# Kernel tuning notes

Measured on AMD Instinct MI355X. Metric: run time of the kernel, lower is better.

The kernel has to match this reference:

```python
import jax, jax.numpy as jnp
import numpy as np

B, S, D, H, WIN = 2, 2048, 1024, 16, 128
DH = D // H


def setup_inputs() -> dict:
    key = jax.random.key(0)
    ks = jax.random.split(key, 6)
    sc = D ** -0.5
    return {
        "x": jax.random.normal(ks[0], (B, S, D), jnp.float32),
        "in_proj_w": jax.random.normal(ks[1], (3 * D, D), jnp.float32) * sc,
        "in_proj_b": jnp.zeros((3 * D,), jnp.float32),
        "out_proj_w": jax.random.normal(ks[2], (D, D), jnp.float32) * sc,
        "out_proj_b": jnp.zeros((D,), jnp.float32),
        "ln1_g": jnp.ones((D,), jnp.float32),
        "ln1_b": jnp.zeros((D,), jnp.float32),
        "spec_wr": jax.random.normal(ks[3], (S // 2 + 1, D), jnp.float32) * 0.02 + 1.0,
        "spec_wi": jax.random.normal(ks[4], (S // 2 + 1, D), jnp.float32) * 0.02,
        "ln2_g": jnp.ones((D,), jnp.float32),
        "ln2_b": jnp.zeros((D,), jnp.float32),
    }


def _layernorm(x, g, b, eps=1e-5):
    mu = jnp.mean(x, axis=-1, keepdims=True)
    var = jnp.mean(jnp.square(x - mu), axis=-1, keepdims=True)
    return (x - mu) * jax.lax.rsqrt(var + eps) * g + b


def reference(x, in_proj_w, in_proj_b, out_proj_w, out_proj_b,
              ln1_g, ln1_b, spec_wr, spec_wi, ln2_g, ln2_b):
    b, s, d = x.shape
    # --- sliding-window MHA (torch nn.MultiheadAttention math) ---
    qkv = x @ in_proj_w.T + in_proj_b            # [B,S,3D]
    q, k, v = jnp.split(qkv, 3, axis=-1)
    q = q.reshape(b, s, H, DH)
    k = k.reshape(b, s, H, DH)
    v = v.reshape(b, s, H, DH)
    scores = jnp.einsum('bqhd,bkhd->bhqk', q, k) * (DH ** -0.5)
    idx = jnp.arange(s)
    band_mask = jnp.abs(idx[:, None] - idx[None, :]) > WIN  # True = masked
    scores = jnp.where(band_mask[None, None], -jnp.inf, scores)
    probs = jax.nn.softmax(scores, axis=-1)
    attn = jnp.einsum('bhqk,bkhd->bqhd', probs, v).reshape(b, s, d)
    attn_out = attn @ out_proj_w.T + out_proj_b
    x_attn = _layernorm(x + attn_out, ln1_g, ln1_b)
    # --- spectral block: rfft along seq, learned complex filter, irfft ---
    Xf = jnp.fft.rfft(x, axis=1)                  # [B, S//2+1, D] complex
    Wc = spec_wr + 1j * spec_wi
    x_wave = jnp.fft.irfft(Xf * Wc[None], n=s, axis=1).astype(x.dtype)
    # --- mix ---
    return _layernorm(x_attn + x_wave, ln2_g, ln2_b)
```

## Files before the change

### kernel.cpp

```cpp
#include <hip/hip_runtime.h>
#include <hip/hip_bf16.h>
#include <math.h>

#define BB    2
#define SS    2048
#define DD    1024
#define HH    16
#define DHH   64
#define WINW  128
#define MROWS (BB * SS)

typedef __attribute__((ext_vector_type(8))) short short8;
typedef __attribute__((ext_vector_type(4))) short short4v;
typedef __attribute__((ext_vector_type(4))) float floatx4;

__device__ __forceinline__ float bf2f(short s) {
  union { unsigned u; float f; } t;
  t.u = ((unsigned)(unsigned short)s) << 16;
  return t.f;
}

__device__ inline void load16_lds(const __hip_bfloat16* g, __hip_bfloat16* l) {
  __builtin_amdgcn_global_load_lds(
      (const __attribute__((address_space(1))) uint32_t*)g,
      (__attribute__((address_space(3))) uint32_t*)l, 16, 0, 0);
}

__global__ __launch_bounds__(256) void prep_fused(
    const float* __restrict__ x, float* __restrict__ xT,
    __hip_bfloat16* __restrict__ x_bf,
    const float* __restrict__ w_in, const float* __restrict__ w_out,
    __hip_bfloat16* __restrict__ w_in_bf, __hip_bfloat16* __restrict__ w_out_bf,
    const float* __restrict__ wr, const float* __restrict__ wi,
    __hip_bfloat16* __restrict__ wrT, __hip_bfloat16* __restrict__ wiT) {
  __shared__ float tile[64][65];
  const int id = blockIdx.x;
  const int tx = threadIdx.x & 63;
  const int ty = threadIdx.x >> 6;

  if (id < 1024) {
    const int bz = id >> 9;
    const int rem = id & 511;
    const int c0 = (rem & 15) * 64;
    const int r0 = (rem >> 4) * 64;
    const size_t base = (size_t)bz * SS * DD;
#pragma unroll
    for (int i = 0; i < 16; ++i) {
      const int r = ty * 16 + i;
      const float v = x[base + (size_t)(r0 + r) * DD + c0 + tx];
      tile[r][tx] = v;
      x_bf[base + (size_t)(r0 + r) * DD + c0 + tx] = __float2bfloat16(v);
    }
    __syncthreads();
#pragma unroll
    for (int i = 0; i < 16; ++i) {
      const int c = ty * 16 + i;
      xT[base + (size_t)(c0 + c) * SS + r0 + tx] = tile[tx][c];
    }
  } else if (id < 2048) {
    const int blk = id - 1024;
    const float* src; __hip_bfloat16* dst; size_t off;
    if (blk < 768) { src = w_in; dst = w_in_bf; off = (size_t)blk * 4096; }
    else { src = w_out; dst = w_out_bf; off = (size_t)(blk - 768) * 4096; }
#pragma unroll
    for (int c = 0; c < 4; ++c) {
      const size_t j = off + c * 1024 + threadIdx.x * 4;
      const float4 v = *(const float4*)(src + j);
      dst[j + 0] = __float2bfloat16(v.x);
      dst[j + 1] = __float2bfloat16(v.y);
      dst[j + 2] = __float2bfloat16(v.z);
      dst[j + 3] = __float2bfloat16(v.w);
    }
  } else {
    const int id2 = id - 2048;
    const int half = id2 >= 272;
    const int rem = id2 - (half ? 272 : 0);
    const float* src = half ? wi : wr;
    __hip_bfloat16* dst = half ? wiT : wrT;
    const int R = 1025, C = DD;
    const int c0 = (rem & 15) * 64;
    const int r0 = (rem >> 4) * 64;
#pragma unroll
    for (int i = 0; i < 16; ++i) {
      const int r = ty * 16 + i;
      if (r0 + r < R) tile[r][tx] = src[(size_t)(r0 + r) * C + c0 + tx];
    }
    __syncthreads();
#pragma unroll
    for (int i = 0; i < 16; ++i) {
      const int c = ty * 16 + i;
      if (r0 + tx < R) dst[(size_t)(c0 + c) * R + r0 + tx] = __float2bfloat16(tile[tx][c]);
    }
  }
}

template <bool BF16OUT>
__device__ __forceinline__ void gemm_tile128(
    const __hip_bfloat16* __restrict__ A, const __hip_bfloat16* __restrict__ B,
    const float* __restrict__ bias, void* __restrict__ Cp,
    int N, int K, int row0, int col0, __hip_bfloat16* sm) {
  __hip_bfloat16* As0 = sm;
  __hip_bfloat16* As1 = sm + 4096;
  __hip_bfloat16* Bs0 = sm + 8192;
  __hip_bfloat16* Bs1 = sm + 12288;
  const int tid  = threadIdx.x;
  const int lane = tid & 63;
  const int wave = tid >> 6;
  const int wrow = (wave >> 1) * 64;
  const int wcol = (wave & 1) * 64;
  const int srow = tid >> 2;
  const int skk  = (tid & 3) * 8;
  const int quad = lane >> 4;
  const int l16  = lane & 15;
  floatx4 acc[4][4] = {};
  for (int k0 = 0; k0 < K; k0 += 64) {
    __syncthreads();
    load16_lds(A + (size_t)(row0 + srow) * K + k0 + skk,           &As0[tid * 8]);
    load16_lds(A + (size_t)(row0 + 64 + srow) * K + k0 + skk,      &As0[2048 + tid * 8]);
    load16_lds(A + (size_t)(row0 + srow) * K + k0 + 32 + skk,      &As1[tid * 8]);
    load16_lds(A + (size_t)(row0 + 64 + srow) * K + k0 + 32 + skk, &As1[2048 + tid * 8]);
    load16_lds(B + (size_t)(col0 + srow) * K + k0 + skk,           &Bs0[tid * 8]);
    load16_lds(B + (size_t)(col0 + 64 + srow) * K + k0 + skk,      &Bs0[2048 + tid * 8]);
    load16_lds(B + (size_t)(col0 + srow) * K + k0 + 32 + skk,      &Bs1[tid * 8]);
    load16_lds(B + (size_t)(col0 + 64 + srow) * K + k0 + 32 + skk, &Bs1[2048 + tid * 8]);
    __syncthreads();
    {
      short8 af[4], bf[4];
#pragma unroll
      for (int i = 0; i < 4; ++i)
        af[i] = *(const short8*)&As0[(wrow + i * 16 + l16) * 32 + quad * 8];
#pragma unroll
      for (int j = 0; j < 4; ++j)
        bf[j] = *(const short8*)&Bs0[(wcol + j * 16 + l16) * 32 + quad * 8];
#pragma unroll
      for (int i = 0; i < 4; ++i)
#pragma unroll
        for (int j = 0; j < 4; ++j)
          acc[i][j] = __builtin_amdgcn_mfma_f32_16x16x32_bf16(af[i], bf[j], acc[i][j], 0, 0, 0);
    }
    {
      short8 af[4], bf[4];
#pragma unroll
      for (int i = 0; i < 4; ++i)
        af[i] = *(const short8*)&As1[(wrow + i * 16 + l16) * 32 + quad * 8];
#pragma unroll
      for (int j = 0; j < 4; ++j)
        bf[j] = *(const short8*)&Bs1[(wcol + j * 16 + l16) * 32 + quad * 8];
#pragma unroll
      for (int i = 0; i < 4; ++i)
#pragma unroll
        for (int j = 0; j < 4; ++j)
          acc[i][j] = __builtin_amdgcn_mfma_f32_16x16x32_bf16(af[i], bf[j], acc[i][j], 0, 0, 0);
    }
  }
#pragma unroll
  for (int i = 0; i < 4; ++i) {
#pragma unroll
    for (int j = 0; j < 4; ++j) {
      const int col = col0 + wcol + j * 16 + l16;
      const float bs = bias[col];
#pragma unroll
      for (int r = 0; r < 4; ++r) {
        const int row = row0 + wrow + i * 16 + quad * 4 + r;
        if (BF16OUT)
          ((__hip_bfloat16*)Cp)[(size_t)row * N + col] = __float2bfloat16(acc[i][j][r] + bs);
        else
          ((float*)Cp)[(size_t)row * N + col] = acc[i][j][r] + bs;
      }
    }
  }
}

#define PAD2(a) ((a) + ((a) >> 5))

__device__ __forceinline__ void spec_body(
    int sid, float* __restrict__ xT,
    const __hip_bfloat16* __restrict__ wrT, const __hip_bfloat16* __restrict__ wiT,
    float* smf) {
  float2* cx  = (float2*)smf;
  float2* twb = cx + 2112;
  float2* twl = twb + 1024;
  const int tid = threadIdx.x;
  const int dpair = sid & 511;
  const int b = sid >> 9;
  const int d0 = dpair * 2, d1 = d0 + 1;
  float* col0 = xT + ((size_t)b * DD + d0) * SS;
  float* col1 = xT + ((size_t)b * DD + d1) * SS;

  for (int s4 = tid * 4; s4 < SS; s4 += 1024) {
    const float4 a = *(const float4*)(col0 + s4);
    const float4 c = *(const float4*)(col1 + s4);
    const int p = PAD2(s4);
    cx[p + 0] = float2{a.x, c.x};
    cx[p + 1] = float2{a.y, c.y};
    cx[p + 2] = float2{a.z, c.z};
    cx[p + 3] = float2{a.w, c.w};
  }
  for (int j = tid; j < 1024; j += 256) {
    float sn, cs;
    __sincosf(-6.283185307179586f * (float)j * (1.0f / 2048.0f), &sn, &cs);
    twb[j] = float2{cs, sn};
  }
#pragma unroll
  for (int s = 1; s <= 9; ++s) {
    const int sz = 1 << (s - 1);
    const float ang = -6.283185307179586f / (float)(1 << s);
    for (int p = tid; p < sz; p += 256) {
      float sn, cs;
      __sincosf(ang * (float)p, &sn, &cs);
      twl[sz - 1 + p] = float2{cs, sn};
    }
  }

  for (int stage = 11; stage >= 1; --stage) {
    __syncthreads();
    const int half = 1 << (stage - 1);
    const float2* twp = (stage >= 10) ? twb : (twl + (half - 1));
    const int tmul = (stage == 10) ? 2 : 1;
#pragma unroll 2
    for (int t = tid; t < SS / 2; t += 256) {
      const int gI = t >> (stage - 1);
      const int p = t & (half - 1);
      const int i = (gI << stage) + p;
      const int j = i + half;
      const float2 w = twp[p * tmul];
      const int ii = PAD2(i), jj = PAD2(j);
      const float2 a = cx[ii];
      const float2 bv = cx[jj];
      cx[ii] = float2{a.x + bv.x, a.y + bv.y};
      const float dr = a.x - bv.x, di = a.y - bv.y;
      cx[jj] = float2{dr * w.x - di * w.y, dr * w.y + di * w.x};
    }
  }
  __syncthreads();

  const __hip_bfloat16* w0r = wrT + (size_t)d0 * 1025;
  const __hip_bfloat16* w0i = wiT + (size_t)d0 * 1025;
  const __hip_bfloat16* w1r = wrT + (size_t)d1 * 1025;
  const __hip_bfloat16* w1i = wiT + (size_t)d1 * 1025;
  const float sc = 1.0f / (float)SS;
  for (int k = tid; k < 1024; k += 256) {
    if (k == 0) {
      const float2 z0 = cx[0];
      cx[0] = float2{z0.x * __bfloat162float(w0r[0]) * sc,
                     z0.y * __bfloat162float(w1r[0]) * sc};
      const float2 zn = cx[1];
      cx[1] = float2{zn.x * __bfloat162float(w0r[1024]) * sc,
                     zn.y * __bfloat162float(w1r[1024]) * sc};
    } else {
      const int p1 = PAD2(__brev((unsigned)k) >> 21);
      const int p2 = PAD2(__brev((unsigned)(SS - k)) >> 21);
      const float2 A = cx[p1];
      const float2 Bv = cx[p2];
      const float z0r = 0.5f * (A.x + Bv.x), z0i = 0.5f * (A.y - Bv.y);
      const float z1r = 0.5f * (A.y + Bv.y), z1i = -0.5f * (A.x - Bv.x);
      const float a0 = __bfloat162float(w0r[k]) * sc, b0 = __bfloat162float(w0i[k]) * sc;
      const float a1 = __bfloat162float(w1r[k]) * sc, b1 = __bfloat162float(w1i[k]) * sc;
      const float y0r = z0r * a0 - z0i * b0, y0i = z0r * b0 + z0i * a0;
      const float y1r = z1r * a1 - z1i * b1, y1i = z1r * b1 + z1i * a1;
      cx[p1] = float2{y0r - y1i, y0i + y1r};
      cx[p2] = float2{y0r + y1i, y1r - y0i};
    }
  }

  for (int stage = 1; stage <= 11; ++stage) {
    __syncthreads();
    const int half = 1 << (stage - 1);
    const float2* twp = (stage >= 10) ? twb : (twl + (half - 1));
    const int tmul = (stage == 10) ? 2 : 1;
#pragma unroll 2
    for (int t = tid; t < SS / 2; t += 256) {
      const int gI = t >> (stage - 1);
      const int p = t & (half - 1);
      const int i = (gI << stage) + p;
      const int j = i + half;
      const float2 w = twp[p * tmul];
      const int ii = PAD2(i), jj = PAD2(j);
      const float2 bv = cx[jj];
      const float tr = bv.x * w.x + bv.y * w.y;
      const float ti = bv.y * w.x - bv.x * w.y;
      const float2 a = cx[ii];
      cx[ii] = float2{a.x + tr, a.y + ti};
      cx[jj] = float2{a.x - tr, a.y - ti};
    }
  }
  __syncthreads();

  for (int s4 = tid * 4; s4 < SS; s4 += 1024) {
    const int p = PAD2(s4);
    float4 a, c;
    const float2 v0 = cx[p + 0], v1 = cx[p + 1], v2 = cx[p + 2], v3 = cx[p + 3];
    a.x = v0.x; a.y = v1.x; a.z = v2.x; a.w = v3.x;
    c.x = v0.y; c.y = v1.y; c.z = v2.y; c.w = v3.y;
    *(float4*)(col0 + s4) = a;
    *(float4*)(col1 + s4) = c;
  }
}

__global__ __launch_bounds__(256) void gemm1_spec(
    const __hip_bfloat16* __restrict__ x_bf, const __hip_bfloat16* __restrict__ w_in_bf,
    const float* __restrict__ in_b, __hip_bfloat16* __restrict__ qkv_bf,
    float* __restrict__ xT, const __hip_bfloat16* __restrict__ wrT,
    const __hip_bfloat16* __restrict__ wiT) {
  extern __shared__ __align__(16) char smem[];
  if (blockIdx.x < 768) {
    const int id = blockIdx.x;
    const int col0 = (id % 24) * 128;
    const int row0 = (id / 24) * 128;
    gemm_tile128<true>(x_bf, w_in_bf, in_b, qkv_bf, 3 * DD, DD, row0, col0,
                       (__hip_bfloat16*)smem);
  } else {
    spec_body(blockIdx.x - 768, xT, wrT, wiT, (float*)smem);
  }
}

__global__ __launch_bounds__(256) void gemm2_tback(
    const __hip_bfloat16* __restrict__ attn_bf, const __hip_bfloat16* __restrict__ w_out_bf,
    const float* __restrict__ out_b, __hip_bfloat16* __restrict__ attn_out_bf,
    const float* __restrict__ xT, __hip_bfloat16* __restrict__ x_wave_bf) {
  extern __shared__ __align__(16) char smem[];
  if (blockIdx.x < 256) {
    const int id = blockIdx.x;
    const int col0 = (id % 8) * 128;
    const int row0 = (id / 8) * 128;
    gemm_tile128<true>(attn_bf, w_out_bf, out_b, attn_out_bf, DD, DD, row0, col0,
                       (__hip_bfloat16*)smem);
  } else {
    float (*tile)[65] = (float(*)[65])smem;
    const int id = blockIdx.x - 256;
    const int bz = id >> 9;
    const int rem = id & 511;
    const int s0 = (rem >> 4) * 64;
    const int d0 = (rem & 15) * 64;
    const int tx = threadIdx.x & 63;
    const int ty = threadIdx.x >> 6;
    const float* src = xT + (size_t)bz * DD * SS;
    __hip_bfloat16* dst = x_wave_bf + (size_t)bz * SS * DD;
#pragma unroll
    for (int i = 0; i < 16; ++i) {
      const int r = ty * 16 + i;
      tile[r][tx] = src[(size_t)(d0 + r) * SS + s0 + tx];
    }
    __syncthreads();
#pragma unroll
    for (int i = 0; i < 16; ++i) {
      const int c = ty * 16 + i;
      dst[(size_t)(s0 + c) * DD + d0 + tx] = __float2bfloat16(tile[tx][c]);
    }
  }
}

__global__ __launch_bounds__(256, 2) void attn_mfma(
    const __hip_bfloat16* __restrict__ qkv, __hip_bfloat16* __restrict__ attn) {
  __shared__ __attribute__((aligned(16))) __hip_bfloat16 QsA[64 * 32];
  __shared__ __attribute__((aligned(16))) __hip_bfloat16 QsB[64 * 32];
  __shared__ __attribute__((aligned(16))) __hip_bfloat16 KsA[160 * 32];
  __shared__ __attribute__((aligned(16))) __hip_bfloat16 KsB[160 * 32];
  __shared__ __attribute__((aligned(16))) __hip_bfloat16 Vt[64 * 168];
  __shared__ __attribute__((aligned(16))) __hip_bfloat16 Ps[64 * 168];

  const int tid  = threadIdx.x;
  const int lane = tid & 63;
  const int w    = tid >> 6;
  const int quad = lane >> 4;
  const int l16  = lane & 15;
  const int q0   = blockIdx.x * 64;
  const int h    = blockIdx.y;
  const int b    = blockIdx.z;
  const int kbase = q0 - WINW;

  const int r_ = tid >> 2;
  const int c8 = (tid & 3) * 8;

  {
    const __hip_bfloat16* src = qkv + ((size_t)(b * SS + q0 + r_)) * (3 * DD) + h * DHH;
    load16_lds(src + c8,      &QsA[r_ * 32 + c8]);
    load16_lds(src + 32 + c8, &QsB[r_ * 32 + c8]);
  }

  short8 qf0, qf1;
  float m_run[4] = {-1e30f, -1e30f, -1e30f, -1e30f};
  float l_run[4] = {0.f, 0.f, 0.f, 0.f};
  floatx4 ob[4] = {};

  for (int c = 0; c < 2; ++c) {
    const int ck0 = kbase + c * 160;
    __syncthreads();
#pragma unroll
    for (int it = 0; it < 3; ++it) {
      const int r = it * 64 + r_;
      if (r < 160) {
        int key = ck0 + r; key = key < 0 ? 0 : (key > SS - 1 ? SS - 1 : key);
        const __hip_bfloat16* src = qkv + ((size_t)(b * SS + key)) * (3 * DD) + DD + h * DHH;
        load16_lds(src + c8,      &KsA[r * 32 + c8]);
        load16_lds(src + 32 + c8, &KsB[r * 32 + c8]);
      }
    }
    {
      const int k4 = (tid >> 3) * 4;
      const int d8 = (tid & 7) * 8;
#pragma unroll
      for (int it = 0; it < 2; ++it) {
        const int rr = it * 128 + k4;
        if (rr < 160) {
          short8 v[4];
#pragma unroll
          for (int u = 0; u < 4; ++u) {
            int key = ck0 + rr + u; key = key < 0 ? 0 : (key > SS - 1 ? SS - 1 : key);
            v[u] = *(const short8*)(qkv + ((size_t)(b * SS + key)) * (3 * DD) + 2 * DD + h * DHH + d8);
          }
#pragma unroll
          for (int j = 0; j < 8; ++j) {
            short4v pk; pk[0] = v[0][j]; pk[1] = v[1][j]; pk[2] = v[2][j]; pk[3] = v[3][j];
            *(short4v*)&Vt[(d8 + j) * 168 + rr] = pk;
          }
        }
      }
    }
    __syncthreads();

    if (c == 0) {
      qf0 = *(const short8*)&QsA[(w * 16 + l16) * 32 + quad * 8];
      qf1 = *(const short8*)&QsB[(w * 16 + l16) * 32 + quad * 8];
    }

    floatx4 sc[10];
#pragma unroll
    for (int kt = 0; kt < 10; ++kt) {
      const short8 bk0 = *(const short8*)&KsA[(kt * 16 + l16) * 32 + quad * 8];
      const short8 bk1 = *(const short8*)&KsB[(kt * 16 + l16) * 32 + quad * 8];
      floatx4 a = {};
      a = __builtin_amdgcn_mfma_f32_16x16x32_bf16(qf0, bk0, a, 0, 0, 0);
      a = __builtin_amdgcn_mfma_f32_16x16x32_bf16(qf1, bk1, a, 0, 0, 0);
      sc[kt] = a;
    }

    float cm[4] = {-1e30f, -1e30f, -1e30f, -1e30f};
#pragma unroll
    for (int kt = 0; kt < 10; ++kt) {
      const int key = ck0 + kt * 16 + l16;
#pragma unroll
      for (int r = 0; r < 4; ++r) {
        const int qq = q0 + w * 16 + quad * 4 + r;
        const int dqk = qq - key;
        const bool ok = (key >= 0) & (key < SS) & (dqk <= WINW) & (dqk >= -WINW);
        const float s = ok ? sc[kt][r] * 0.125f : -1e30f;
        sc[kt][r] = s;
        cm[r] = fmaxf(cm[r], s);
      }
    }
#pragma unroll
    for (int off = 1; off < 16; off <<= 1)
#pragma unroll
      for (int r = 0; r < 4; ++r) cm[r] = fmaxf(cm[r], __shfl_xor(cm[r], off, 64));

    float alpha[4], csum[4] = {0.f, 0.f, 0.f, 0.f};
#pragma unroll
    for (int r = 0; r < 4; ++r) {
      const float mn = fmaxf(m_run[r], cm[r]);
      alpha[r] = __expf(m_run[r] - mn);
      m_run[r] = mn;
    }

    __hip_bfloat16* Pw = &Ps[w * 16 * 168];
#pragma unroll
    for (int kt = 0; kt < 10; ++kt) {
#pragma unroll
      for (int r = 0; r < 4; ++r) {
        const float p = __expf(sc[kt][r] - m_run[r]);
        csum[r] += p;
        Pw[(quad * 4 + r) * 168 + kt * 16 + l16] = __float2bfloat16(p);
      }
    }
#pragma unroll
    for (int off = 1; off < 16; off <<= 1)
#pragma unroll
      for (int r = 0; r < 4; ++r) csum[r] += __shfl_xor(csum[r], off, 64);
#pragma unroll
    for (int r = 0; r < 4; ++r) l_run[r] = l_run[r] * alpha[r] + csum[r];
#pragma unroll
    for (int t = 0; t < 4; ++t)
#pragma unroll
      for (int r = 0; r < 4; ++r) ob[t][r] *= alpha[r];

#pragma unroll
    for (int kt = 0; kt < 5; ++kt) {
      const short8 pf = *(const short8*)&Pw[l16 * 168 + kt * 32 + quad * 8];
#pragma unroll
      for (int t = 0; t < 4; ++t) {
        const short8 vf = *(const short8*)&Vt[(t * 16 + l16) * 168 + kt * 32 + quad * 8];
        ob[t] = __builtin_amdgcn_mfma_f32_16x16x32_bf16(pf, vf, ob[t], 0, 0, 0);
      }
    }
  }

  float inv[4];
#pragma unroll
  for (int r = 0; r < 4; ++r) inv[r] = 1.f / l_run[r];
  const int qq0 = q0 + w * 16 + quad * 4;
#pragma unroll
  for (int t = 0; t < 4; ++t)
#pragma unroll
    for (int r = 0; r < 4; ++r)
      attn[((size_t)(b * SS + qq0 + r)) * DD + h * DHH + t * 16 + l16] =
          __float2bfloat16(ob[t][r] * inv[r]);
}

__global__ __launch_bounds__(256) void ln_fused(
    const float* __restrict__ x, const __hip_bfloat16* __restrict__ attn_out,
    const float* __restrict__ g1, const float* __restrict__ b1,
    const __hip_bfloat16* __restrict__ xwave,
    const float* __restrict__ g2, const float* __restrict__ b2,
    float* __restrict__ out) {
  const int row = blockIdx.x;
  const int tid = threadIdx.x;
  const int lane = tid & 63;
  const int wave = tid >> 6;
  __shared__ float red[8];

  const float4 xv = *(const float4*)(x + (size_t)row * DD + tid * 4);
  const short4v av = *(const short4v*)(attn_out + (size_t)row * DD + tid * 4);
  float v[4] = {xv.x + bf2f(av[0]), xv.y + bf2f(av[1]),
                xv.z + bf2f(av[2]), xv.w + bf2f(av[3])};

  float s = v[0] + v[1] + v[2] + v[3];
  float s2 = v[0] * v[0] + v[1] * v[1] + v[2] * v[2] + v[3] * v[3];
#pragma unroll
  for (int off = 32; off; off >>= 1) {
    s += __shfl_xor(s, off, 64);
    s2 += __shfl_xor(s2, off, 64);
  }
  if (lane == 0) { red[wave] = s; red[4 + wave] = s2; }
  __syncthreads();
  s = red[0] + red[1] + red[2] + red[3];
  s2 = red[4] + red[5] + red[6] + red[7];
  float mu = s * (1.f / DD);
  float var = s2 * (1.f / DD) - mu * mu;
  float r = rsqrtf(var + 1e-5f);

  const float4 g1v = *(const float4*)(g1 + tid * 4);
  const float4 b1v = *(const float4*)(b1 + tid * 4);
  const short4v wv = *(const short4v*)(xwave + (size_t)row * DD + tid * 4);
  float a[4];
  a[0] = (v[0] - mu) * r * g1v.x + b1v.x + bf2f(wv[0]);
  a[1] = (v[1] - mu) * r * g1v.y + b1v.y + bf2f(wv[1]);
  a[2] = (v[2] - mu) * r * g1v.z + b1v.z + bf2f(wv[2]);
  a[3] = (v[3] - mu) * r * g1v.w + b1v.w + bf2f(wv[3]);

  s = a[0] + a[1] + a[2] + a[3];
  s2 = a[0] * a[0] + a[1] * a[1] + a[2] * a[2] + a[3] * a[3];
#pragma unroll
  for (int off = 32; off; off >>= 1) {
    s += __shfl_xor(s, off, 64);
    s2 += __shfl_xor(s2, off, 64);
  }
  __syncthreads();
  if (lane == 0) { red[wave] = s; red[4 + wave] = s2; }
  __syncthreads();
  s = red[0] + red[1] + red[2] + red[3];
  s2 = red[4] + red[5] + red[6] + red[7];
  mu = s * (1.f / DD);
  var = s2 * (1.f / DD) - mu * mu;
  r = rsqrtf(var + 1e-5f);

  const float4 g2v = *(const float4*)(g2 + tid * 4);
  const float4 b2v = *(const float4*)(b2 + tid * 4);
  float4 o;
  o.x = (a[0] - mu) * r * g2v.x + b2v.x;
  o.y = (a[1] - mu) * r * g2v.y + b2v.y;
  o.z = (a[2] - mu) * r * g2v.z + b2v.z;
  o.w = (a[3] - mu) * r * g2v.w + b2v.w;
  *(float4*)(out + (size_t)row * DD + tid * 4) = o;
}

extern "C" void kernel_launch(void* const* d_in, const int* in_sizes, int n_in,
                              void* d_out, int out_size, void* d_ws, size_t ws_size,
                              hipStream_t stream) {
  const float* x     = (const float*)d_in[0];
  const float* in_w  = (const float*)d_in[1];
  const float* in_b  = (const float*)d_in[2];
  const float* out_w = (const float*)d_in[3];
  const float* out_b = (const float*)d_in[4];
  const float* ln1_g = (const float*)d_in[5];
  const float* ln1_b = (const float*)d_in[6];
  const float* wr    = (const float*)d_in[7];
  const float* wi    = (const float*)d_in[8];
  const float* ln2_g = (const float*)d_in[9];
  const float* ln2_b = (const float*)d_in[10];
  float* out = (float*)d_out;

  char* ws = (char*)d_ws;
  float* xT                = (float*)(ws);
  __hip_bfloat16* x_bf     = (__hip_bfloat16*)(ws + 16777216);
  __hip_bfloat16* attn_bf  = (__hip_bfloat16*)(ws + 16777216);
  __hip_bfloat16* w_in_bf  = (__hip_bfloat16*)(ws + 25165824);
  __hip_bfloat16* w_out_bf = (__hip_bfloat16*)(ws + 31457280);
  __hip_bfloat16* qkv_bf   = (__hip_bfloat16*)(ws + 33554432);
  __hip_bfloat16* attn_out_bf = (__hip_bfloat16*)(ws + 33554432);
  __hip_bfloat16* x_wave_bf   = (__hip_bfloat16*)(ws + 44040192);
  __hip_bfloat16* wrT      = (__hip_bfloat16*)(ws + 58720256);
  __hip_bfloat16* wiT      = (__hip_bfloat16*)(ws + 60819456);

  prep_fused<<<2592, 256, 0, stream>>>(x, xT, x_bf, in_w, out_w,
                                       w_in_bf, w_out_bf, wr, wi, wrT, wiT);

  gemm1_spec<<<1792, 256, 32768, stream>>>(x_bf, w_in_bf, in_b, qkv_bf,
                                           xT, wrT, wiT);

  attn_mfma<<<dim3(SS / 64, HH, BB), 256, 0, stream>>>(qkv_bf, attn_bf);

  gemm2_tback<<<1280, 256, 32768, stream>>>(attn_bf, w_out_bf, out_b,
                                            attn_out_bf, xT, x_wave_bf);

  ln_fused<<<MROWS, 256, 0, stream>>>(x, attn_out_bf, ln1_g, ln1_b,
                                      x_wave_bf, ln2_g, ln2_b, out);
}
```

Measured before the change: 228.7 us.

## Store transposed spectral buffer in bf16 and use radix-4 FFT with inline twiddles

```diff
diff --git a/kernel.cpp b/kernel.cpp
--- a/kernel.cpp
+++ b/kernel.cpp
@@ -27,7 +27,7 @@
 }
 
 __global__ __launch_bounds__(256) void prep_fused(
-    const float* __restrict__ x, float* __restrict__ xT,
+    const float* __restrict__ x, __hip_bfloat16* __restrict__ xT_bf,
     __hip_bfloat16* __restrict__ x_bf,
     const float* __restrict__ w_in, const float* __restrict__ w_out,
     __hip_bfloat16* __restrict__ w_in_bf, __hip_bfloat16* __restrict__ w_out_bf,
@@ -55,7 +55,7 @@
 #pragma unroll
     for (int i = 0; i < 16; ++i) {
       const int c = ty * 16 + i;
-      xT[base + (size_t)(c0 + c) * SS + r0 + tx] = tile[tx][c];
+      xT_bf[base + (size_t)(c0 + c) * SS + r0 + tx] = __float2bfloat16(tile[tx][c]);
     }
   } else if (id < 2048) {
     const int blk = id - 1024;
@@ -174,63 +174,62 @@
 #define PAD2(a) ((a) + ((a) >> 5))
 
 __device__ __forceinline__ void spec_body(
-    int sid, float* __restrict__ xT,
+    int sid, __hip_bfloat16* __restrict__ xw,
     const __hip_bfloat16* __restrict__ wrT, const __hip_bfloat16* __restrict__ wiT,
     float* smf) {
-  float2* cx  = (float2*)smf;
-  float2* twb = cx + 2112;
-  float2* twl = twb + 1024;
+  float2* cx = (float2*)smf;
   const int tid = threadIdx.x;
   const int dpair = sid & 511;
   const int b = sid >> 9;
   const int d0 = dpair * 2, d1 = d0 + 1;
-  float* col0 = xT + ((size_t)b * DD + d0) * SS;
-  float* col1 = xT + ((size_t)b * DD + d1) * SS;
+  __hip_bfloat16* col0 = xw + ((size_t)b * DD + d0) * SS;
+  __hip_bfloat16* col1 = xw + ((size_t)b * DD + d1) * SS;
 
   for (int s4 = tid * 4; s4 < SS; s4 += 1024) {
-    const float4 a = *(const float4*)(col0 + s4);
-    const float4 c = *(const float4*)(col1 + s4);
+    const short4v a = *(const short4v*)(col0 + s4);
+    const short4v c = *(const short4v*)(col1 + s4);
     const int p = PAD2(s4);
-    cx[p + 0] = float2{a.x, c.x};
-    cx[p + 1] = float2{a.y, c.y};
-    cx[p + 2] = float2{a.z, c.z};
-    cx[p + 3] = float2{a.w, c.w};
-  }
-  for (int j = tid; j < 1024; j += 256) {
-    float sn, cs;
-    __sincosf(-6.283185307179586f * (float)j * (1.0f / 2048.0f), &sn, &cs);
-    twb[j] = float2{cs, sn};
-  }
-#pragma unroll
-  for (int s = 1; s <= 9; ++s) {
-    const int sz = 1 << (s - 1);
+    cx[p + 0] = float2{bf2f(a[0]), bf2f(c[0])};
+    cx[p + 1] = float2{bf2f(a[1]), bf2f(c[1])};
+    cx[p + 2] = float2{bf2f(a[2]), bf2f(c[2])};
+    cx[p + 3] = float2{bf2f(a[3]), bf2f(c[3])};
+  }
+
+#pragma unroll
+  for (int s = 11; s >= 3; s -= 2) {
+    __syncthreads();
+    const int h2 = 1 << (s - 2);
     const float ang = -6.283185307179586f / (float)(1 << s);
-    for (int p = tid; p < sz; p += 256) {
-      float sn, cs;
-      __sincosf(ang * (float)p, &sn, &cs);
-      twl[sz - 1 + p] = float2{cs, sn};
-    }
-  }
-
-  for (int stage = 11; stage >= 1; --stage) {
-    __syncthreads();
-    const int half = 1 << (stage - 1);
-    const float2* twp = (stage >= 10) ? twb : (twl + (half - 1));
-    const int tmul = (stage == 10) ? 2 : 1;
 #pragma unroll 2
-    for (int t = tid; t < SS / 2; t += 256) {
-      const int gI = t >> (stage - 1);
-      const int p = t & (half - 1);
-      const int i = (gI << stage) + p;
-      const int j = i + half;
-      const float2 w = twp[p * tmul];
-      const int ii = PAD2(i), jj = PAD2(j);
-      const float2 a = cx[ii];
-      const float2 bv = cx[jj];
-      cx[ii] = float2{a.x + bv.x, a.y + bv.y};
-      const float dr = a.x - bv.x, di = a.y - bv.y;
-      cx[jj] = float2{dr * w.x - di * w.y, dr * w.y + di * w.x};
-    }
+    for (int g = tid; g < 512; g += 256) {
+      const int q = g & (h2 - 1);
+      const int base = ((g >> (s - 2)) << s) + q;
+      const int i0 = PAD2(base), i1 = PAD2(base + h2);
+      const int i2 = PAD2(base + 2 * h2), i3 = PAD2(base + 3 * h2);
+      float sn, cn;
+      __sincosf(ang * (float)q, &sn, &cn);
+      const float2 A = cx[i0], B = cx[i1], C = cx[i2], D = cx[i3];
+      const float2 Ap = {A.x + C.x, A.y + C.y};
+      const float acx = A.x - C.x, acy = A.y - C.y;
+      const float2 Cp = {acx * cn - acy * sn, acx * sn + acy * cn};
+      const float2 Bp = {B.x + D.x, B.y + D.y};
+      const float bdx = B.x - D.x, bdy = B.y - D.y;
+      const float2 Dp = {bdx * sn + bdy * cn, bdy * sn - bdx * cn};
+      const float w3r = cn * cn - sn * sn, w3i = 2.f * cn * sn;
+      cx[i0] = float2{Ap.x + Bp.x, Ap.y + Bp.y};
+      const float abx = Ap.x - Bp.x, aby = Ap.y - Bp.y;
+      cx[i1] = float2{abx * w3r - aby * w3i, abx * w3i + aby * w3r};
+      cx[i2] = float2{Cp.x + Dp.x, Cp.y + Dp.y};
+      const float cdx = Cp.x - Dp.x, cdy = Cp.y - Dp.y;
+      cx[i3] = float2{cdx * w3r - cdy * w3i, cdx * w3i + cdy * w3r};
+    }
+  }
+  __syncthreads();
+  for (int t = tid; t < 1024; t += 256) {
+    const int i = PAD2(2 * t), j = PAD2(2 * t + 1);
+    const float2 a = cx[i], b = cx[j];
+    cx[i] = float2{a.x + b.x, a.y + b.y};
+    cx[j] = float2{a.x - b.x, a.y - b.y};
   }
   __syncthreads();
 
@@ -263,44 +262,70 @@
     }
   }
 
-  for (int stage = 1; stage <= 11; ++stage) {
-    __syncthreads();
-    const int half = 1 << (stage - 1);
-    const float2* twp = (stage >= 10) ? twb : (twl + (half - 1));
-    const int tmul = (stage == 10) ? 2 : 1;
+#pragma unroll
+  for (int s = 1; s <= 9; s += 2) {
+    __syncthreads();
+    const int h = 1 << (s - 1);
+    const float ang = -6.283185307179586f / (float)(1 << (s + 1));
 #pragma unroll 2
-    for (int t = tid; t < SS / 2; t += 256) {
-      const int gI = t >> (stage - 1);
-      const int p = t & (half - 1);
-      const int i = (gI << stage) + p;
-      const int j = i + half;
-      const float2 w = twp[p * tmul];
-      const int ii = PAD2(i), jj = PAD2(j);
-      const float2 bv = cx[jj];
-      const float tr = bv.x * w.x + bv.y * w.y;
-      const float ti = bv.y * w.x - bv.x * w.y;
-      const float2 a = cx[ii];
-      cx[ii] = float2{a.x + tr, a.y + ti};
-      cx[jj] = float2{a.x - tr, a.y - ti};
-    }
+    for (int g = tid; g < 512; g += 256) {
+      const int q = g & (h - 1);
+      const int base = ((g >> (s - 1)) << (s + 1)) + q;
+      const int i0 = PAD2(base), i1 = PAD2(base + h);
+      const int i2 = PAD2(base + 2 * h), i3 = PAD2(base + 3 * h);
+      float sn, cn;
+      __sincosf(ang * (float)q, &sn, &cn);
+      const float wpr = cn, wpi = -sn;
+      const float wsr = cn * cn - sn * sn, wsi = -2.f * cn * sn;
+      const float2 A = cx[i0], B = cx[i1], C = cx[i2], D = cx[i3];
+      const float2 tB = {B.x * wsr - B.y * wsi, B.x * wsi + B.y * wsr};
+      const float2 tD = {D.x * wsr - D.y * wsi, D.x * wsi + D.y * wsr};
+      const float2 Ap = {A.x + tB.x, A.y + tB.y};
+      const float2 Bp = {A.x - tB.x, A.y - tB.y};
+      const float2 Cp = {C.x + tD.x, C.y + tD.y};
+      const float2 Dp = {C.x - tD.x, C.y - tD.y};
+      const float2 u = {Cp.x * wpr - Cp.y * wpi, Cp.x * wpi + Cp.y * wpr};
+      const float2 v = {Dp.x * sn - Dp.y * cn, Dp.x * cn + Dp.y * sn};
+      cx[i0] = float2{Ap.x + u.x, Ap.y + u.y};
+      cx[i2] = float2{Ap.x - u.x, Ap.y - u.y};
+      cx[i1] = float2{Bp.x + v.x, Bp.y + v.y};
+      cx[i3] = float2{Bp.x - v.x, Bp.y - v.y};
+    }
+  }
+  __syncthreads();
+  for (int p = tid; p < 1024; p += 256) {
+    float sn, cn;
+    __sincosf(-6.283185307179586f * (float)p * (1.0f / 2048.0f), &sn, &cn);
+    const int i = PAD2(p), j = PAD2(p + 1024);
+    const float2 a = cx[i], b = cx[j];
+    const float tr = b.x * cn + b.y * sn;
+    const float ti = b.y * cn - b.x * sn;
+    cx[i] = float2{a.x + tr, a.y + ti};
+    cx[j] = float2{a.x - tr, a.y - ti};
   }
   __syncthreads();
 
   for (int s4 = tid * 4; s4 < SS; s4 += 1024) {
     const int p = PAD2(s4);
-    float4 a, c;
     const float2 v0 = cx[p + 0], v1 = cx[p + 1], v2 = cx[p + 2], v3 = cx[p + 3];
-    a.x = v0.x; a.y = v1.x; a.z = v2.x; a.w = v3.x;
-    c.x = v0.y; c.y = v1.y; c.z = v2.y; c.w = v3.y;
-    *(float4*)(col0 + s4) = a;
-    *(float4*)(col1 + s4) = c;
+    short4v a, c;
+    a[0] = (short)__bfloat16_as_ushort(__float2bfloat16(v0.x));
+    a[1] = (short)__bfloat16_as_ushort(__float2bfloat16(v1.x));
+    a[2] = (short)__bfloat16_as_ushort(__float2bfloat16(v2.x));
+    a[3] = (short)__bfloat16_as_ushort(__float2bfloat16(v3.x));
+    c[0] = (short)__bfloat16_as_ushort(__float2bfloat16(v0.y));
+    c[1] = (short)__bfloat16_as_ushort(__float2bfloat16(v1.y));
+    c[2] = (short)__bfloat16_as_ushort(__float2bfloat16(v2.y));
+    c[3] = (short)__bfloat16_as_ushort(__float2bfloat16(v3.y));
+    *(short4v*)(col0 + s4) = a;
+    *(short4v*)(col1 + s4) = c;
   }
 }
 
 __global__ __launch_bounds__(256) void gemm1_spec(
     const __hip_bfloat16* __restrict__ x_bf, const __hip_bfloat16* __restrict__ w_in_bf,
     const float* __restrict__ in_b, __hip_bfloat16* __restrict__ qkv_bf,
-    float* __restrict__ xT, const __hip_bfloat16* __restrict__ wrT,
+    __hip_bfloat16* __restrict__ xT_bf, const __hip_bfloat16* __restrict__ wrT,
     const __hip_bfloat16* __restrict__ wiT) {
   extern __shared__ __align__(16) char smem[];
   if (blockIdx.x < 768) {
@@ -310,14 +335,14 @@
     gemm_tile128<true>(x_bf, w_in_bf, in_b, qkv_bf, 3 * DD, DD, row0, col0,
                        (__hip_bfloat16*)smem);
   } else {
-    spec_body(blockIdx.x - 768, xT, wrT, wiT, (float*)smem);
+    spec_body(blockIdx.x - 768, xT_bf, wrT, wiT, (float*)smem);
   }
 }
 
 __global__ __launch_bounds__(256) void gemm2_tback(
     const __hip_bfloat16* __restrict__ attn_bf, const __hip_bfloat16* __restrict__ w_out_bf,
     const float* __restrict__ out_b, __hip_bfloat16* __restrict__ attn_out_bf,
-    const float* __restrict__ xT, __hip_bfloat16* __restrict__ x_wave_bf) {
+    const __hip_bfloat16* __restrict__ xT_bf, __hip_bfloat16* __restrict__ x_wave_bf) {
   extern __shared__ __align__(16) char smem[];
   if (blockIdx.x < 256) {
     const int id = blockIdx.x;
@@ -334,12 +359,12 @@
     const int d0 = (rem & 15) * 64;
     const int tx = threadIdx.x & 63;
     const int ty = threadIdx.x >> 6;
-    const float* src = xT + (size_t)bz * DD * SS;
+    const __hip_bfloat16* src = xT_bf + (size_t)bz * DD * SS;
     __hip_bfloat16* dst = x_wave_bf + (size_t)bz * SS * DD;
 #pragma unroll
     for (int i = 0; i < 16; ++i) {
       const int r = ty * 16 + i;
-      tile[r][tx] = src[(size_t)(d0 + r) * SS + s0 + tx];
+      tile[r][tx] = __bfloat162float(src[(size_t)(d0 + r) * SS + s0 + tx]);
     }
     __syncthreads();
 #pragma unroll
@@ -590,7 +615,7 @@
   float* out = (float*)d_out;
 
   char* ws = (char*)d_ws;
-  float* xT                = (float*)(ws);
+  __hip_bfloat16* xT_bf    = (__hip_bfloat16*)(ws);
   __hip_bfloat16* x_bf     = (__hip_bfloat16*)(ws + 16777216);
   __hip_bfloat16* attn_bf  = (__hip_bfloat16*)(ws + 16777216);
   __hip_bfloat16* w_in_bf  = (__hip_bfloat16*)(ws + 25165824);
@@ -601,16 +626,16 @@
   __hip_bfloat16* wrT      = (__hip_bfloat16*)(ws + 58720256);
   __hip_bfloat16* wiT      = (__hip_bfloat16*)(ws + 60819456);
 
-  prep_fused<<<2592, 256, 0, stream>>>(x, xT, x_bf, in_w, out_w,
+  prep_fused<<<2592, 256, 0, stream>>>(x, xT_bf, x_bf, in_w, out_w,
                                        w_in_bf, w_out_bf, wr, wi, wrT, wiT);
 
   gemm1_spec<<<1792, 256, 32768, stream>>>(x_bf, w_in_bf, in_b, qkv_bf,
-                                           xT, wrT, wiT);
+                                           xT_bf, wrT, wiT);
 
   attn_mfma<<<dim3(SS / 64, HH, BB), 256, 0, stream>>>(qkv_bf, attn_bf);
 
   gemm2_tback<<<1280, 256, 32768, stream>>>(attn_bf, w_out_bf, out_b,
-                                            attn_out_bf, xT, x_wave_bf);
+                                            attn_out_bf, xT_bf, x_wave_bf);
 
   ln_fused<<<MROWS, 256, 0, stream>>>(x, attn_out_bf, ln1_g, ln1_b,
                                       x_wave_bf, ln2_g, ln2_b, out);
```

After: 215.6 us. 5.7% less time.
